# Kernel tuning notes

Hardware: AMD Instinct MI355X
Metric: run time of the kernel (lower is better)

Reference implementation:

```python
import jax, jax.numpy as jnp
import numpy as np

N_NODES = 100000
N_EDGES = 1600000
D = 64
N_LAYERS = 3


def setup_inputs() -> dict:
    key = jax.random.key(0)
    k1, k2, k3, k4 = jax.random.split(key, 4)
    x = jax.random.normal(k1, (N_NODES, D), dtype=jnp.float32)
    edge_index = jax.random.randint(k2, (2, N_EDGES), 0, N_NODES, dtype=jnp.int64)
    scale = 1.0 / np.sqrt(D)
    Wl = jax.random.normal(k3, (N_LAYERS, D, D), dtype=jnp.float32) * scale
    Wr = jax.random.normal(k4, (N_LAYERS, D, D), dtype=jnp.float32) * scale
    b = jnp.zeros((N_LAYERS, D), dtype=jnp.float32)
    return {"x": x, "edge_index": edge_index, "Wl": Wl, "Wr": Wr, "b": b}


def _sage_conv(x, src, dst, Wl, Wr, b, n_nodes):
    # mean-aggregate source features onto targets, then two linear maps
    msgs = x[src]                                              # [E, d]
    summed = jax.ops.segment_sum(msgs, dst, num_segments=n_nodes)   # [N, d]
    cnt = jax.ops.segment_sum(jnp.ones(src.shape[0], x.dtype), dst,
                              num_segments=n_nodes)            # [N]
    agg = summed / jnp.maximum(cnt, 1.0)[:, None]
    return agg @ Wl + x @ Wr + b


def reference(x, edge_index, Wl, Wr, b):
    # GraphSAGE forward in eval mode (dropout is identity, p=0.5 only in training)
    src, dst = edge_index[0], edge_index[1]
    n = x.shape[0]
    h = x
    for i in range(N_LAYERS - 1):
        h = _sage_conv(h, src, dst, Wl[i], Wr[i], b[i], n)
        h = jax.nn.relu(h)
    h = _sage_conv(h, src, dst, Wl[-1], Wr[-1], b[-1], n)
    return h
```

## Files before the change

### kernel.cpp

```cpp
#include <hip/hip_runtime.h>
#include <hip/hip_fp16.h>

#define DD 64
#define NPB 32
#define EPC 8192
#define BK_SHIFT 8
#define BNODES 256
#define SCHUNK 1024
#define APAD 136

typedef _Float16 half8 __attribute__((ext_vector_type(8)));
typedef float f32x4 __attribute__((ext_vector_type(4)));

union U8 { uint2 u; __half2 h[2]; };

__global__ __launch_bounds__(256) void f32_to_f16_kernel(const float* __restrict__ in,
                                                         __half* __restrict__ out, int n8) {
    int i = blockIdx.x * blockDim.x + threadIdx.x;
    if (i < n8) {
        const float4* p = reinterpret_cast<const float4*>(in + (size_t)i * 8);
        float4 a = p[0], b = p[1];
        __half2* q = reinterpret_cast<__half2*>(out + (size_t)i * 8);
        q[0] = __floats2half2_rn(a.x, a.y);
        q[1] = __floats2half2_rn(a.z, a.w);
        q[2] = __floats2half2_rn(b.x, b.y);
        q[3] = __floats2half2_rn(b.z, b.w);
    }
}

__global__ __launch_bounds__(256) void wswz_kernel(const float* __restrict__ Wl,
                                                   const float* __restrict__ Wr,
                                                   __half* __restrict__ Wswz, int nlayer) {
    int idx = blockIdx.x * 256 + threadIdx.x;
    int total = nlayer * 4 * 4 * 64;
    if (idx >= total) return;
    int lane = idx & 63;
    int nt   = (idx >> 6) & 3;
    int kt   = (idx >> 8) & 3;
    int L    = idx >> 10;
    int n     = nt * 16 + (lane & 15);
    int kbase = kt * 32 + 8 * (lane >> 4);
    __half* o = Wswz + (size_t)idx * 8;
#pragma unroll
    for (int i = 0; i < 8; ++i) {
        int k = kbase + i;
        float v = (k < 64) ? Wl[(size_t)L * 4096 + (size_t)k * 64 + n]
                           : Wr[(size_t)L * 4096 + (size_t)(k - 64) * 64 + n];
        o[i] = __float2half(v);
    }
}

__global__ __launch_bounds__(256) void binA_kernel(const int* __restrict__ dst, int e, int nc,
                                                   int* __restrict__ histT, int nbuck) {
    __shared__ int h[512];
    int tid = threadIdx.x, c = blockIdx.x;
    for (int i = tid; i < nbuck; i += 256) h[i] = 0;
    __syncthreads();
    int base = c * EPC;
#pragma unroll
    for (int j = 0; j < EPC / 256; ++j) {
        int i = base + j * 256 + tid;
        if (i < e) atomicAdd(&h[dst[i] >> BK_SHIFT], 1);
    }
    __syncthreads();
    for (int b = tid; b < nbuck; b += 256) histT[b * nc + c] = h[b];
}

__global__ __launch_bounds__(256) void scan_part_kernel(const int* __restrict__ data, int tot,
                                                        int* __restrict__ blocksum) {
    __shared__ int red[256];
    int tid = threadIdx.x;
    int base = blockIdx.x * SCHUNK + tid * 4;
    int s = 0;
#pragma unroll
    for (int j = 0; j < 4; ++j) {
        int i = base + j;
        if (i < tot) s += data[i];
    }
    red[tid] = s;
    __syncthreads();
    for (int off = 128; off > 0; off >>= 1) {
        if (tid < off) red[tid] += red[tid + off];
        __syncthreads();
    }
    if (tid == 0) blocksum[blockIdx.x] = red[0];
}

__global__ __launch_bounds__(1024) void scan_mid_kernel(int* __restrict__ blocksum, int nb) {
    __shared__ int sc[1024];
    int tid = threadIdx.x;
    int v = (tid < nb) ? blocksum[tid] : 0;
    sc[tid] = v;
    __syncthreads();
    for (int off = 1; off < 1024; off <<= 1) {
        int t = (tid >= off) ? sc[tid - off] : 0;
        __syncthreads();
        sc[tid] += t;
        __syncthreads();
    }
    if (tid < nb) blocksum[tid] = sc[tid] - v;
}

__global__ __launch_bounds__(256) void scan_write_kernel(int* __restrict__ data, int tot,
                                                         const int* __restrict__ blockoff) {
    __shared__ int sc[256];
    int tid = threadIdx.x;
    int base = blockIdx.x * SCHUNK + tid * 4;
    int e0 = 0, e1 = 0, e2 = 0, e3 = 0;
    if (base + 0 < tot) e0 = data[base + 0];
    if (base + 1 < tot) e1 = data[base + 1];
    if (base + 2 < tot) e2 = data[base + 2];
    if (base + 3 < tot) e3 = data[base + 3];
    int s = e0 + e1 + e2 + e3;
    sc[tid] = s;
    __syncthreads();
    for (int off = 1; off < 256; off <<= 1) {
        int t = (tid >= off) ? sc[tid - off] : 0;
        __syncthreads();
        sc[tid] += t;
        __syncthreads();
    }
    int run = blockoff[blockIdx.x] + sc[tid] - s;
    if (base + 0 < tot) data[base + 0] = run;
    if (base + 1 < tot) data[base + 1] = run + e0;
    if (base + 2 < tot) data[base + 2] = run + e0 + e1;
    if (base + 3 < tot) data[base + 3] = run + e0 + e1 + e2;
}

__global__ __launch_bounds__(256) void binB_kernel(const int* __restrict__ src, const int* __restrict__ dst,
                                                   int e, int nc, const int* __restrict__ offT,
                                                   int nbuck, int* __restrict__ binned) {
    __shared__ int cur[512];
    int tid = threadIdx.x, c = blockIdx.x;
    for (int b = tid; b < nbuck; b += 256) cur[b] = offT[b * nc + c];
    __syncthreads();
    int base = c * EPC;
#pragma unroll
    for (int j = 0; j < EPC / 256; ++j) {
        int i = base + j * 256 + tid;
        if (i < e) {
            int d = dst[i];
            int p = atomicAdd(&cur[d >> BK_SHIFT], 1);
            binned[p] = (unsigned)(d & (BNODES - 1)) << 24 | (unsigned)src[i];
        }
    }
}

__global__ __launch_bounds__(BNODES) void place_kernel(const int* __restrict__ binned,
                                                       const int* __restrict__ offT, int nc,
                                                       int nbuck, int e, int n,
                                                       int* __restrict__ rowp, int* __restrict__ esrc) {
    __shared__ int deg[BNODES];
    __shared__ int sc[BNODES];
    int tid = threadIdx.x, b = blockIdx.x;
    int node0 = b << BK_SHIFT;
    int base = offT[b * nc];
    int end  = (b + 1 < nbuck) ? offT[(b + 1) * nc] : e;
    deg[tid] = 0;
    __syncthreads();
    for (int i = base + tid; i < end; i += BNODES)
        atomicAdd(&deg[(unsigned)binned[i] >> 24], 1);
    __syncthreads();
    int v = deg[tid];
    sc[tid] = v;
    __syncthreads();
    for (int off = 1; off < BNODES; off <<= 1) {
        int t = (tid >= off) ? sc[tid - off] : 0;
        __syncthreads();
        sc[tid] += t;
        __syncthreads();
    }
    int excl = sc[tid] - v;
    int node = node0 + tid;
    if (node < n) rowp[node] = base + excl;
    if (b == 0 && tid == 0) rowp[n] = e;
    deg[tid] = base + excl;
    __syncthreads();
    for (int i = base + tid; i < end; i += BNODES) {
        int p = binned[i];
        int pos = atomicAdd(&deg[(unsigned)p >> 24], 1);
        esrc[pos] = p & 0xFFFFFF;
    }
}

__global__ __launch_bounds__(512) void sage_layer_kernel(
    const __half* __restrict__ hin16, const float* __restrict__ self32,
    const int* __restrict__ rowp, const int* __restrict__ esrc,
    const __half* __restrict__ Bfrag,
    const float* __restrict__ bias,
    float* __restrict__ out32, __half* __restrict__ out16,
    int n, int relu)
{
    __shared__ _Float16 sA[NPB][APAD];

    int tid = threadIdx.x;
    int grp = tid >> 4;
    int l   = tid & 15;
    int node = blockIdx.x * NPB + grp;

    if (node < n) {
        if (self32) {
            float4 h4 = *reinterpret_cast<const float4*>(self32 + (size_t)node * DD + l * 4);
            U8 pk; pk.h[0] = __floats2half2_rn(h4.x, h4.y); pk.h[1] = __floats2half2_rn(h4.z, h4.w);
            *reinterpret_cast<uint2*>(&sA[grp][64 + 4 * l]) = pk.u;
        } else {
            uint2 v = *reinterpret_cast<const uint2*>(hin16 + (size_t)node * DD + l * 4);
            *reinterpret_cast<uint2*>(&sA[grp][64 + 4 * l]) = v;
        }

        int beg = rowp[node], end = rowp[node + 1];
        float ax = 0.f, ay = 0.f, az = 0.f, aw = 0.f;
        int t = beg;
        for (; t + 8 <= end; t += 8) {
            int s0 = esrc[t + 0], s1 = esrc[t + 1], s2 = esrc[t + 2], s3 = esrc[t + 3];
            int s4 = esrc[t + 4], s5 = esrc[t + 5], s6 = esrc[t + 6], s7 = esrc[t + 7];
            U8 v0, v1, v2, v3, v4, v5, v6, v7;
            v0.u = *reinterpret_cast<const uint2*>(hin16 + (size_t)s0 * DD + l * 4);
            v1.u = *reinterpret_cast<const uint2*>(hin16 + (size_t)s1 * DD + l * 4);
            v2.u = *reinterpret_cast<const uint2*>(hin16 + (size_t)s2 * DD + l * 4);
            v3.u = *reinterpret_cast<const uint2*>(hin16 + (size_t)s3 * DD + l * 4);
            v4.u = *reinterpret_cast<const uint2*>(hin16 + (size_t)s4 * DD + l * 4);
            v5.u = *reinterpret_cast<const uint2*>(hin16 + (size_t)s5 * DD + l * 4);
            v6.u = *reinterpret_cast<const uint2*>(hin16 + (size_t)s6 * DD + l * 4);
            v7.u = *reinterpret_cast<const uint2*>(hin16 + (size_t)s7 * DD + l * 4);
            float2 a0 = __half22float2(v0.h[0]), b0 = __half22float2(v0.h[1]);
            float2 a1 = __half22float2(v1.h[0]), b1 = __half22float2(v1.h[1]);
            float2 a2 = __half22float2(v2.h[0]), b2 = __half22float2(v2.h[1]);
            float2 a3 = __half22float2(v3.h[0]), b3 = __half22float2(v3.h[1]);
            float2 a4 = __half22float2(v4.h[0]), b4 = __half22float2(v4.h[1]);
            float2 a5 = __half22float2(v5.h[0]), b5 = __half22float2(v5.h[1]);
            float2 a6 = __half22float2(v6.h[0]), b6 = __half22float2(v6.h[1]);
            float2 a7 = __half22float2(v7.h[0]), b7 = __half22float2(v7.h[1]);
            ax += ((a0.x + a1.x) + (a2.x + a3.x)) + ((a4.x + a5.x) + (a6.x + a7.x));
            ay += ((a0.y + a1.y) + (a2.y + a3.y)) + ((a4.y + a5.y) + (a6.y + a7.y));
            az += ((b0.x + b1.x) + (b2.x + b3.x)) + ((b4.x + b5.x) + (b6.x + b7.x));
            aw += ((b0.y + b1.y) + (b2.y + b3.y)) + ((b4.y + b5.y) + (b6.y + b7.y));
        }
        if (t + 4 <= end) {
            int s0 = esrc[t + 0], s1 = esrc[t + 1], s2 = esrc[t + 2], s3 = esrc[t + 3];
            U8 v0, v1, v2, v3;
            v0.u = *reinterpret_cast<const uint2*>(hin16 + (size_t)s0 * DD + l * 4);
            v1.u = *reinterpret_cast<const uint2*>(hin16 + (size_t)s1 * DD + l * 4);
            v2.u = *reinterpret_cast<const uint2*>(hin16 + (size_t)s2 * DD + l * 4);
            v3.u = *reinterpret_cast<const uint2*>(hin16 + (size_t)s3 * DD + l * 4);
            float2 a0 = __half22float2(v0.h[0]), b0 = __half22float2(v0.h[1]);
            float2 a1 = __half22float2(v1.h[0]), b1 = __half22float2(v1.h[1]);
            float2 a2 = __half22float2(v2.h[0]), b2 = __half22float2(v2.h[1]);
            float2 a3 = __half22float2(v3.h[0]), b3 = __half22float2(v3.h[1]);
            ax += (a0.x + a1.x) + (a2.x + a3.x);
            ay += (a0.y + a1.y) + (a2.y + a3.y);
            az += (b0.x + b1.x) + (b2.x + b3.x);
            aw += (b0.y + b1.y) + (b2.y + b3.y);
            t += 4;
        }
        for (; t < end; ++t) {
            int s = esrc[t];
            U8 v; v.u = *reinterpret_cast<const uint2*>(hin16 + (size_t)s * DD + l * 4);
            float2 f0 = __half22float2(v.h[0]), f1 = __half22float2(v.h[1]);
            ax += f0.x; ay += f0.y; az += f1.x; aw += f1.y;
        }
        float inv = 1.0f / fmaxf((float)(end - beg), 1.0f);
        U8 pk; pk.h[0] = __floats2half2_rn(ax * inv, ay * inv);
               pk.h[1] = __floats2half2_rn(az * inv, aw * inv);
        *reinterpret_cast<uint2*>(&sA[grp][4 * l]) = pk.u;
    }
    __syncthreads();

    int wave  = tid >> 6;
    int lane  = tid & 63;
    int mtile = wave >> 2;
    int nt    = wave & 3;
    int arow  = mtile * 16 + (lane & 15);
    f32x4 acc = {0.f, 0.f, 0.f, 0.f};
    const half8* bfr = reinterpret_cast<const half8*>(Bfrag);
#pragma unroll
    for (int kt = 0; kt < 4; ++kt) {
        half8 a = *reinterpret_cast<const half8*>(&sA[arow][kt * 32 + 8 * (lane >> 4)]);
        half8 b = bfr[(kt * 4 + nt) * 64 + lane];
        acc = __builtin_amdgcn_mfma_f32_16x16x32_f16(a, b, acc, 0, 0, 0);
    }
    int col = nt * 16 + (lane & 15);
    float bv = bias[col];
    int rbase = blockIdx.x * NPB + mtile * 16 + (lane >> 4) * 4;
#pragma unroll
    for (int j = 0; j < 4; ++j) {
        int r = rbase + j;
        if (r < n) {
            float o = acc[j] + bv;
            if (relu) o = fmaxf(o, 0.f);
            if (out32) out32[(size_t)r * DD + col] = o;
            if (out16) out16[(size_t)r * DD + col] = __float2half(o);
        }
    }
}

extern "C" void kernel_launch(void* const* d_in, const int* in_sizes, int n_in,
                              void* d_out, int out_size, void* d_ws, size_t ws_size,
                              hipStream_t stream) {
    (void)n_in; (void)out_size; (void)ws_size;
    const float* x  = (const float*)d_in[0];
    const int*   ei = (const int*)d_in[1];
    const float* Wl = (const float*)d_in[2];
    const float* Wr = (const float*)d_in[3];
    const float* bb = (const float*)d_in[4];
    float* out = (float*)d_out;

    int n = in_sizes[0] / DD;
    int e = in_sizes[1] / 2;
    const int* src = ei;
    const int* dst = ei + e;

    int nc    = (e + EPC - 1) / EPC;
    int nbuck = (n + BNODES - 1) >> BK_SHIFT;
    int tot   = nbuck * nc;
    int nsb   = (tot + SCHUNK - 1) / SCHUNK;

    char* cur = (char*)d_ws;
    auto alloc = [&](size_t bytes) -> void* {
        void* p = (void*)cur;
        cur += (bytes + 255) & ~(size_t)255;
        return p;
    };
    int*    histT  = (int*)alloc((size_t)tot * 4);
    int*    bsum   = (int*)alloc(1024 * 4);
    int*    binned = (int*)alloc((size_t)e * 4);
    int*    rowp   = (int*)alloc(((size_t)n + 1) * 4);
    int*    esrc   = (int*)alloc((size_t)e * 4);
    __half* x16    = (__half*)alloc((size_t)n * DD * 2);
    __half* hA16   = (__half*)alloc((size_t)n * DD * 2);
    __half* hB16   = (__half*)alloc((size_t)n * DD * 2);
    __half* Wswz   = (__half*)alloc((size_t)3 * 8192 * 2);

    int n8 = n * DD / 8;
    f32_to_f16_kernel<<<(n8 + 255) / 256, 256, 0, stream>>>(x, x16, n8);
    wswz_kernel<<<(3 * 4 * 4 * 64 + 255) / 256, 256, 0, stream>>>(Wl, Wr, Wswz, 3);

    binA_kernel<<<nc, 256, 0, stream>>>(dst, e, nc, histT, nbuck);
    scan_part_kernel<<<nsb, 256, 0, stream>>>(histT, tot, bsum);
    scan_mid_kernel<<<1, 1024, 0, stream>>>(bsum, nsb);
    scan_write_kernel<<<nsb, 256, 0, stream>>>(histT, tot, bsum);
    binB_kernel<<<nc, 256, 0, stream>>>(src, dst, e, nc, histT, nbuck, binned);
    place_kernel<<<nbuck, BNODES, 0, stream>>>(binned, histT, nc, nbuck, e, n, rowp, esrc);

    int lb = (n + NPB - 1) / NPB;
    sage_layer_kernel<<<lb, 512, 0, stream>>>(x16,  x,       rowp, esrc, Wswz,         bb,          nullptr, hA16, n, 1);
    sage_layer_kernel<<<lb, 512, 0, stream>>>(hA16, nullptr, rowp, esrc, Wswz + 8192,  bb + DD,     nullptr, hB16, n, 1);
    sage_layer_kernel<<<lb, 512, 0, stream>>>(hB16, nullptr, rowp, esrc, Wswz + 16384, bb + 2 * DD, out,     nullptr, n, 0);
}
```

Measured before the change: 190.4 us.

## Merge prep kernels into one launch and widen destination buckets to 512 nodes

Three independent preprocessing kernels (fp32-to-fp16 conversion, weight swizzle, destination histogram) are merged into a single launch that dispatches on block index. This removes two kernel launches and the serialization gaps between them. Separately, buckets now cover 512 nodes instead of 256, which halves the bucket count and shrinks the histogram and scan work. The place kernel now runs 512-thread blocks, and the packed source index drops from 24 to 23 bits, which still fits 100k nodes.

```diff
diff --git a/kernel.cpp b/kernel.cpp
--- a/kernel.cpp
+++ b/kernel.cpp
@@ -4,8 +4,8 @@
 #define DD 64
 #define NPB 32
 #define EPC 8192
-#define BK_SHIFT 8
-#define BNODES 256
+#define BK_SHIFT 9
+#define BNODES 512
 #define SCHUNK 1024
 #define APAD 136
 
@@ -14,56 +14,56 @@
 
 union U8 { uint2 u; __half2 h[2]; };
 
-__global__ __launch_bounds__(256) void f32_to_f16_kernel(const float* __restrict__ in,
-                                                         __half* __restrict__ out, int n8) {
-    int i = blockIdx.x * blockDim.x + threadIdx.x;
-    if (i < n8) {
-        const float4* p = reinterpret_cast<const float4*>(in + (size_t)i * 8);
-        float4 a = p[0], b = p[1];
-        __half2* q = reinterpret_cast<__half2*>(out + (size_t)i * 8);
-        q[0] = __floats2half2_rn(a.x, a.y);
-        q[1] = __floats2half2_rn(a.z, a.w);
-        q[2] = __floats2half2_rn(b.x, b.y);
-        q[3] = __floats2half2_rn(b.z, b.w);
-    }
-}
-
-__global__ __launch_bounds__(256) void wswz_kernel(const float* __restrict__ Wl,
-                                                   const float* __restrict__ Wr,
-                                                   __half* __restrict__ Wswz, int nlayer) {
-    int idx = blockIdx.x * 256 + threadIdx.x;
-    int total = nlayer * 4 * 4 * 64;
-    if (idx >= total) return;
-    int lane = idx & 63;
-    int nt   = (idx >> 6) & 3;
-    int kt   = (idx >> 8) & 3;
-    int L    = idx >> 10;
-    int n     = nt * 16 + (lane & 15);
-    int kbase = kt * 32 + 8 * (lane >> 4);
-    __half* o = Wswz + (size_t)idx * 8;
-#pragma unroll
-    for (int i = 0; i < 8; ++i) {
-        int k = kbase + i;
-        float v = (k < 64) ? Wl[(size_t)L * 4096 + (size_t)k * 64 + n]
-                           : Wr[(size_t)L * 4096 + (size_t)(k - 64) * 64 + n];
-        o[i] = __float2half(v);
-    }
-}
-
-__global__ __launch_bounds__(256) void binA_kernel(const int* __restrict__ dst, int e, int nc,
-                                                   int* __restrict__ histT, int nbuck) {
-    __shared__ int h[512];
-    int tid = threadIdx.x, c = blockIdx.x;
-    for (int i = tid; i < nbuck; i += 256) h[i] = 0;
-    __syncthreads();
-    int base = c * EPC;
-#pragma unroll
-    for (int j = 0; j < EPC / 256; ++j) {
-        int i = base + j * 256 + tid;
-        if (i < e) atomicAdd(&h[dst[i] >> BK_SHIFT], 1);
-    }
-    __syncthreads();
-    for (int b = tid; b < nbuck; b += 256) histT[b * nc + c] = h[b];
+__global__ __launch_bounds__(256) void prep_kernel(
+    const float* __restrict__ x, __half* __restrict__ x16, int n8, int nconvb,
+    const int* __restrict__ dst, int e, int nc, int* __restrict__ histT, int nbuck,
+    const float* __restrict__ Wl, const float* __restrict__ Wr, __half* __restrict__ Wswz)
+{
+    __shared__ int h[BNODES];
+    int bid = blockIdx.x, tid = threadIdx.x;
+    if (bid < nconvb) {
+        int i = bid * 256 + tid;
+        if (i < n8) {
+            const float4* p = reinterpret_cast<const float4*>(x + (size_t)i * 8);
+            float4 a = p[0], b = p[1];
+            __half2* q = reinterpret_cast<__half2*>(x16 + (size_t)i * 8);
+            q[0] = __floats2half2_rn(a.x, a.y);
+            q[1] = __floats2half2_rn(a.z, a.w);
+            q[2] = __floats2half2_rn(b.x, b.y);
+            q[3] = __floats2half2_rn(b.z, b.w);
+        }
+    } else if (bid < nconvb + nc) {
+        int c = bid - nconvb;
+        for (int i = tid; i < nbuck; i += 256) h[i] = 0;
+        __syncthreads();
+        int base = c * EPC;
+#pragma unroll
+        for (int j = 0; j < EPC / 256; ++j) {
+            int i = base + j * 256 + tid;
+            if (i < e) atomicAdd(&h[dst[i] >> BK_SHIFT], 1);
+        }
+        __syncthreads();
+        for (int b = tid; b < nbuck; b += 256) histT[b * nc + c] = h[b];
+    } else {
+        int idx = (bid - nconvb - nc) * 256 + tid;
+        int total = 3 * 4 * 4 * 64;
+        if (idx < total) {
+            int lane = idx & 63;
+            int nt   = (idx >> 6) & 3;
+            int kt   = (idx >> 8) & 3;
+            int L    = idx >> 10;
+            int nn    = nt * 16 + (lane & 15);
+            int kbase = kt * 32 + 8 * (lane >> 4);
+            __half* o = Wswz + (size_t)idx * 8;
+#pragma unroll
+            for (int i = 0; i < 8; ++i) {
+                int k = kbase + i;
+                float v = (k < 64) ? Wl[(size_t)L * 4096 + (size_t)k * 64 + nn]
+                                   : Wr[(size_t)L * 4096 + (size_t)(k - 64) * 64 + nn];
+                o[i] = __float2half(v);
+            }
+        }
+    }
 }
 
 __global__ __launch_bounds__(256) void scan_part_kernel(const int* __restrict__ data, int tot,
@@ -130,7 +130,7 @@
 __global__ __launch_bounds__(256) void binB_kernel(const int* __restrict__ src, const int* __restrict__ dst,
                                                    int e, int nc, const int* __restrict__ offT,
                                                    int nbuck, int* __restrict__ binned) {
-    __shared__ int cur[512];
+    __shared__ int cur[BNODES];
     int tid = threadIdx.x, c = blockIdx.x;
     for (int b = tid; b < nbuck; b += 256) cur[b] = offT[b * nc + c];
     __syncthreads();
@@ -141,7 +141,7 @@
         if (i < e) {
             int d = dst[i];
             int p = atomicAdd(&cur[d >> BK_SHIFT], 1);
-            binned[p] = (unsigned)(d & (BNODES - 1)) << 24 | (unsigned)src[i];
+            binned[p] = (int)(((unsigned)(d & (BNODES - 1)) << 23) | (unsigned)src[i]);
         }
     }
 }
@@ -159,7 +159,7 @@
     deg[tid] = 0;
     __syncthreads();
     for (int i = base + tid; i < end; i += BNODES)
-        atomicAdd(&deg[(unsigned)binned[i] >> 24], 1);
+        atomicAdd(&deg[(unsigned)binned[i] >> 23], 1);
     __syncthreads();
     int v = deg[tid];
     sc[tid] = v;
@@ -178,8 +178,8 @@
     __syncthreads();
     for (int i = base + tid; i < end; i += BNODES) {
         int p = binned[i];
-        int pos = atomicAdd(&deg[(unsigned)p >> 24], 1);
-        esrc[pos] = p & 0xFFFFFF;
+        int pos = atomicAdd(&deg[(unsigned)p >> 23], 1);
+        esrc[pos] = p & 0x7FFFFF;
     }
 }
 
@@ -331,11 +331,12 @@
     __half* hB16   = (__half*)alloc((size_t)n * DD * 2);
     __half* Wswz   = (__half*)alloc((size_t)3 * 8192 * 2);
 
-    int n8 = n * DD / 8;
-    f32_to_f16_kernel<<<(n8 + 255) / 256, 256, 0, stream>>>(x, x16, n8);
-    wswz_kernel<<<(3 * 4 * 4 * 64 + 255) / 256, 256, 0, stream>>>(Wl, Wr, Wswz, 3);
-
-    binA_kernel<<<nc, 256, 0, stream>>>(dst, e, nc, histT, nbuck);
+    int n8     = n * DD / 8;
+    int nconvb = (n8 + 255) / 256;
+    int nwswzb = (3 * 4 * 4 * 64 + 255) / 256;
+    prep_kernel<<<nconvb + nc + nwswzb, 256, 0, stream>>>(
+        x, x16, n8, nconvb, dst, e, nc, histT, nbuck, Wl, Wr, Wswz);
+
     scan_part_kernel<<<nsb, 256, 0, stream>>>(histT, tot, bsum);
     scan_mid_kernel<<<1, 1024, 0, stream>>>(bsum, nsb);
     scan_write_kernel<<<nsb, 256, 0, stream>>>(histT, tot, bsum);
```

After: 185.4 us. 2.6% less time.
